# Kernel optimization log

Hardware: AMD Instinct MI355X
Metric: run time of the kernel (lower is better)

The kernel has to match this reference:

```python
import jax, jax.numpy as jnp
import numpy as np

N_TOKENS = 1_000_000
NUM_FEATURES = 128
NUM_CLUSTERS = 64


def setup_inputs() -> dict:
    key = jax.random.key(0)
    kx, kc = jax.random.split(key)
    x = jax.random.normal(kx, (1, N_TOKENS, NUM_FEATURES), dtype=jnp.float32)
    # learned parameter, initialized as torch.randn(num_clusters, num_features)
    cluster_centers = jax.random.normal(kc, (NUM_CLUSTERS, NUM_FEATURES), dtype=jnp.float32)
    return {"x": x, "cluster_centers": cluster_centers}


def reference(x, cluster_centers):
    # x: (1, n, d); cluster_centers: (k, d)
    # O(n*k*d) broadcast intermediate of the original). argmin is identical
    # to argmin over torch.norm since sqrt is monotone.
    x2 = jnp.sum(x * x, axis=-1)                                  # (1, n)
    c2 = jnp.sum(cluster_centers * cluster_centers, axis=-1)      # (k,)
    xc = jnp.einsum('bnd,kd->bnk', x, cluster_centers)            # (1, n, k)
    d2 = x2[..., None] + c2[None, None, :] - 2.0 * xc             # (1, n, k)
    # nearest token index for each cluster (min over the token dim)
    indices = jnp.argmin(d2, axis=1)                              # (1, k)
    # gather the selected token features: (1, k, d)
    selected = x[:, indices[0], :]
    return selected
```

## Files before the change

### kernel.cpp

```cpp
#include <hip/hip_runtime.h>
#include <math.h>

#define NTOK   1000000
#define NFEAT  128
#define NCLUS  64
#define TT     256
#define KC     16
#define NCHUNK (NFEAT / KC)
#define XPAD   260
#define NTILES ((NTOK + TT - 1) / TT)
#define GRID_P 768

__global__ void zero_ctr_kernel(int* ctr) { *ctr = 0; }

__global__ __launch_bounds__(256, 3)
void cluster_part_kernel(const float* __restrict__ x, const float* __restrict__ cc,
                         int* __restrict__ ctr,
                         float* __restrict__ pv, int* __restrict__ pi)
{
    __shared__ float cs[NFEAT][NCLUS];
    __shared__ float xs[KC][XPAD];
    __shared__ float x2s[TT];
    __shared__ float c2s[NCLUS];
    __shared__ int   tileno;

    const int tid = threadIdx.x;
    const int cg  = tid & 7;
    const int tg  = tid >> 3;
    const int l   = tid & 3;
    const int g   = tid >> 2;

    {
        float s = 0.f;
        const float* src = cc + (long)g * NFEAT + l * 4;
        #pragma unroll
        for (int r = 0; r < 8; ++r) {
            float4 v = *(const float4*)(src + r * 16);
            const int f = r * 16 + l * 4;
            cs[f + 0][g] = v.x; cs[f + 1][g] = v.y;
            cs[f + 2][g] = v.z; cs[f + 3][g] = v.w;
            s = fmaf(v.x, v.x, s); s = fmaf(v.y, v.y, s);
            s = fmaf(v.z, v.z, s); s = fmaf(v.w, v.w, s);
        }
        s += __shfl_xor(s, 1);
        s += __shfl_xor(s, 2);
        if (l == 0) c2s[g] = s;
    }
    __syncthreads();

    float c2r[8];
    #pragma unroll
    for (int j = 0; j < 8; ++j) c2r[j] = c2s[cg * 8 + j];

    float bestv[8]; int besti[8];
    #pragma unroll
    for (int j = 0; j < 8; ++j) { bestv[j] = INFINITY; besti[j] = 0x7fffffff; }

    for (;;) {
        if (tid == 0) tileno = atomicAdd(ctr, 1);
        __syncthreads();
        const int tile = tileno;
        if (tile >= NTILES) break;
        const long tb = (long)tile * TT;

        float4 pf[4];
        #pragma unroll
        for (int r = 0; r < 4; ++r) {
            long n = tb + r * 64 + g;
            if (n >= NTOK) n = NTOK - 1;
            pf[r] = *(const float4*)(x + n * NFEAT + l * 4);
        }

        float acc[8][8];
        #pragma unroll
        for (int i = 0; i < 8; ++i)
            #pragma unroll
            for (int j = 0; j < 8; ++j) acc[i][j] = 0.f;
        float x2a[4] = {0.f, 0.f, 0.f, 0.f};

        #pragma unroll 1
        for (int kc = 0; kc < NCHUNK; ++kc) {
            __syncthreads();
            #pragma unroll
            for (int r = 0; r < 4; ++r) {
                float4 v = pf[r];
                const int row = r * 64 + g;
                xs[l * 4 + 0][row] = v.x; xs[l * 4 + 1][row] = v.y;
                xs[l * 4 + 2][row] = v.z; xs[l * 4 + 3][row] = v.w;
                x2a[r] = fmaf(v.x, v.x, x2a[r]);
                x2a[r] = fmaf(v.y, v.y, x2a[r]);
                x2a[r] = fmaf(v.z, v.z, x2a[r]);
                x2a[r] = fmaf(v.w, v.w, x2a[r]);
            }
            if (kc + 1 < NCHUNK) {
                #pragma unroll
                for (int r = 0; r < 4; ++r) {
                    long n = tb + r * 64 + g;
                    if (n >= NTOK) n = NTOK - 1;
                    pf[r] = *(const float4*)(x + n * NFEAT + (kc + 1) * KC + l * 4);
                }
            }
            __syncthreads();

            const int kb = kc * KC;
            #pragma unroll 4
            for (int k = 0; k < KC; ++k) {
                float4 xa = *(const float4*)&xs[k][tg * 8];
                float4 xb = *(const float4*)&xs[k][tg * 8 + 4];
                float4 ca = *(const float4*)&cs[kb + k][cg * 8];
                float4 cb = *(const float4*)&cs[kb + k][cg * 8 + 4];
                float xv[8] = {xa.x, xa.y, xa.z, xa.w, xb.x, xb.y, xb.z, xb.w};
                float cv[8] = {ca.x, ca.y, ca.z, ca.w, cb.x, cb.y, cb.z, cb.w};
                #pragma unroll
                for (int i = 0; i < 8; ++i)
                    #pragma unroll
                    for (int j = 0; j < 8; ++j)
                        acc[i][j] = fmaf(xv[i], cv[j], acc[i][j]);
            }
        }

        #pragma unroll
        for (int r = 0; r < 4; ++r) {
            float s = x2a[r];
            s += __shfl_xor(s, 1);
            s += __shfl_xor(s, 2);
            if (l == 0) x2s[r * 64 + g] = s;
        }
        __syncthreads();

        #pragma unroll
        for (int i = 0; i < 8; ++i) {
            const long n = tb + tg * 8 + i;
            if (n >= NTOK) continue;
            const float x2 = x2s[tg * 8 + i];
            #pragma unroll
            for (int j = 0; j < 8; ++j) {
                float s = (x2 + c2r[j]) - 2.0f * acc[i][j];
                if (s < bestv[j]) { bestv[j] = s; besti[j] = (int)n; }
            }
        }
    }

    __syncthreads();
    float* rv = &xs[0][0];
    int*   ri = (int*)(&xs[0][0] + 2048);
    #pragma unroll
    for (int j = 0; j < 8; ++j) {
        rv[(cg * 8 + j) * 32 + tg] = bestv[j];
        ri[(cg * 8 + j) * 32 + tg] = besti[j];
    }
    __syncthreads();
    if (tid < NCLUS) {
        float bv = rv[tid * 32]; int bi = ri[tid * 32];
        #pragma unroll
        for (int t = 1; t < 32; ++t) {
            float v = rv[tid * 32 + t]; int ii = ri[tid * 32 + t];
            if (v < bv || (v == bv && ii < bi)) { bv = v; bi = ii; }
        }
        pv[(long)blockIdx.x * NCLUS + tid] = bv;
        pi[(long)blockIdx.x * NCLUS + tid] = bi;
    }
}

__global__ __launch_bounds__(256)
void cluster_final_kernel(const float* __restrict__ x,
                          const float* __restrict__ pv, const int* __restrict__ pi,
                          float* __restrict__ out)
{
    const int c   = blockIdx.x;
    const int tid = threadIdx.x;
    __shared__ float sv[256];
    __shared__ int   si[256];

    float bv = INFINITY; int bi = 0x7fffffff;
    for (int b = tid; b < GRID_P; b += 256) {
        float v = pv[(long)b * NCLUS + c]; int ii = pi[(long)b * NCLUS + c];
        if (v < bv || (v == bv && ii < bi)) { bv = v; bi = ii; }
    }
    sv[tid] = bv; si[tid] = bi;
    __syncthreads();
    for (int s = 128; s > 0; s >>= 1) {
        if (tid < s) {
            float v = sv[tid + s]; int ii = si[tid + s];
            if (v < sv[tid] || (v == sv[tid] && ii < si[tid])) {
                sv[tid] = v; si[tid] = ii;
            }
        }
        __syncthreads();
    }
    const int best = si[0];
    if (tid < NFEAT) out[c * NFEAT + tid] = x[(long)best * NFEAT + tid];
}

extern "C" void kernel_launch(void* const* d_in, const int* in_sizes, int n_in,
                              void* d_out, int out_size, void* d_ws, size_t ws_size,
                              hipStream_t stream) {
    const float* x  = (const float*)d_in[0];
    const float* cc = (const float*)d_in[1];
    float* out = (float*)d_out;

    int*   ctr = (int*)d_ws;
    float* pv  = (float*)((char*)d_ws + 256);
    int*   pi  = (int*)((char*)d_ws + 256 + (size_t)GRID_P * NCLUS * sizeof(float));

    zero_ctr_kernel<<<1, 1, 0, stream>>>(ctr);
    cluster_part_kernel<<<GRID_P, 256, 0, stream>>>(x, cc, ctr, pv, pi);
    cluster_final_kernel<<<NCLUS, 256, 0, stream>>>(x, pv, pi, out);
}
```

Baseline: 729.0 us.

## Compute distances with split-bf16 MFMA and per-wave static token partitioning

Replaces the scalar FP32 FMA outer-product GEMM with bf16 MFMA 32x32x16 instructions. Each operand is split into a high and a low bf16 part, and three MFMAs per step approximate FP32 accuracy. Each wave owns 32-token subtiles assigned statically, with register prefetch of x straight from global memory. This removes the atomic tile counter, the LDS staging of x and the block-level barriers. The cost is extra conversion ALU work and a possible argmin mismatch from the reduced-precision dot products, since the lo*lo term is dropped.

```diff
diff --git a/kernel.cpp b/kernel.cpp
--- a/kernel.cpp
+++ b/kernel.cpp
@@ -4,158 +4,153 @@
 #define NTOK   1000000
 #define NFEAT  128
 #define NCLUS  64
-#define TT     256
-#define KC     16
-#define NCHUNK (NFEAT / KC)
-#define XPAD   260
-#define NTILES ((NTOK + TT - 1) / TT)
-#define GRID_P 768
-
-__global__ void zero_ctr_kernel(int* ctr) { *ctr = 0; }
+#define SUBT   32
+#define NSUB   (NTOK / SUBT)
+#define NBLK   768
+#define NWAVE  (NBLK * 4)
+#define CPAD   136
+
+typedef __attribute__((ext_vector_type(8)))  short bf16x8;
+typedef __attribute__((ext_vector_type(16))) float f32x16;
+
+__device__ __forceinline__ unsigned short f2bf(float f) {
+    unsigned u = __float_as_uint(f);
+    return (unsigned short)((u + 0x7fffu + ((u >> 16) & 1u)) >> 16);
+}
+__device__ __forceinline__ float bf2f(unsigned short h) {
+    return __uint_as_float((unsigned)h << 16);
+}
 
 __global__ __launch_bounds__(256, 3)
 void cluster_part_kernel(const float* __restrict__ x, const float* __restrict__ cc,
-                         int* __restrict__ ctr,
                          float* __restrict__ pv, int* __restrict__ pi)
 {
-    __shared__ float cs[NFEAT][NCLUS];
-    __shared__ float xs[KC][XPAD];
-    __shared__ float x2s[TT];
+    __shared__ unsigned short chi[NCLUS][CPAD];
+    __shared__ unsigned short clo[NCLUS][CPAD];
     __shared__ float c2s[NCLUS];
-    __shared__ int   tileno;
+    __shared__ float rv[512];
+    __shared__ int   ri[512];
 
     const int tid = threadIdx.x;
-    const int cg  = tid & 7;
-    const int tg  = tid >> 3;
-    const int l   = tid & 3;
-    const int g   = tid >> 2;
+    const int l   = tid & 63;
+    const int w   = tid >> 6;
+    const int lr  = l & 31;
+    const int lh  = l >> 5;
 
     {
+        const int cl = tid >> 2, q = tid & 3;
+        const float* src = cc + cl * NFEAT + q * 32;
         float s = 0.f;
-        const float* src = cc + (long)g * NFEAT + l * 4;
         #pragma unroll
         for (int r = 0; r < 8; ++r) {
-            float4 v = *(const float4*)(src + r * 16);
-            const int f = r * 16 + l * 4;
-            cs[f + 0][g] = v.x; cs[f + 1][g] = v.y;
-            cs[f + 2][g] = v.z; cs[f + 3][g] = v.w;
-            s = fmaf(v.x, v.x, s); s = fmaf(v.y, v.y, s);
-            s = fmaf(v.z, v.z, s); s = fmaf(v.w, v.w, s);
+            float4 v = *(const float4*)(src + r * 4);
+            float vv[4] = {v.x, v.y, v.z, v.w};
+            #pragma unroll
+            for (int e = 0; e < 4; ++e) {
+                float f = vv[e];
+                unsigned short h  = f2bf(f);
+                unsigned short lo = f2bf(f - bf2f(h));
+                chi[cl][q * 32 + r * 4 + e] = h;
+                clo[cl][q * 32 + r * 4 + e] = lo;
+                s = fmaf(f, f, s);
+            }
         }
         s += __shfl_xor(s, 1);
         s += __shfl_xor(s, 2);
-        if (l == 0) c2s[g] = s;
+        if (q == 0) c2s[cl] = s;
     }
     __syncthreads();
 
-    float c2r[8];
-    #pragma unroll
-    for (int j = 0; j < 8; ++j) c2r[j] = c2s[cg * 8 + j];
-
-    float bestv[8]; int besti[8];
-    #pragma unroll
-    for (int j = 0; j < 8; ++j) { bestv[j] = INFINITY; besti[j] = 0x7fffffff; }
-
-    for (;;) {
-        if (tid == 0) tileno = atomicAdd(ctr, 1);
-        __syncthreads();
-        const int tile = tileno;
-        if (tile >= NTILES) break;
-        const long tb = (long)tile * TT;
-
-        float4 pf[4];
-        #pragma unroll
-        for (int r = 0; r < 4; ++r) {
-            long n = tb + r * 64 + g;
-            if (n >= NTOK) n = NTOK - 1;
-            pf[r] = *(const float4*)(x + n * NFEAT + l * 4);
-        }
-
-        float acc[8][8];
-        #pragma unroll
-        for (int i = 0; i < 8; ++i)
+    const float c2v0 = c2s[lr];
+    const float c2v1 = c2s[lr + 32];
+
+    float bestv0 = INFINITY, bestv1 = INFINITY;
+    int   besti0 = 0x7fffffff, besti1 = 0x7fffffff;
+
+    const int gw = blockIdx.x * 4 + w;
+
+    float4 pfa[2], pfb[2];
+    {
+        const float* p0 = x + ((long)gw * SUBT + lr) * NFEAT + lh * 8;
+        pfa[0] = *(const float4*)(p0);
+        pfb[0] = *(const float4*)(p0 + 4);
+        pfa[1] = *(const float4*)(p0 + 16);
+        pfb[1] = *(const float4*)(p0 + 20);
+    }
+
+    for (int st = gw; st < NSUB; st += NWAVE) {
+        f32x16 acc0, acc1;
+        #pragma unroll
+        for (int i = 0; i < 16; ++i) { acc0[i] = 0.f; acc1[i] = 0.f; }
+        float x2p = 0.f;
+
+        #pragma unroll
+        for (int ks = 0; ks < 8; ++ks) {
+            float4 a = pfa[ks & 1];
+            float4 b = pfb[ks & 1];
+            {
+                const int ks2 = (ks + 2) & 7;
+                const int st2 = (ks < 6) ? st : st + NWAVE;
+                if (st2 < NSUB) {
+                    const float* p2 = x + ((long)st2 * SUBT + lr) * NFEAT + ks2 * 16 + lh * 8;
+                    pfa[ks & 1] = *(const float4*)(p2);
+                    pfb[ks & 1] = *(const float4*)(p2 + 4);
+                }
+            }
+            float av[8] = {a.x, a.y, a.z, a.w, b.x, b.y, b.z, b.w};
+            bf16x8 ahi, alo;
             #pragma unroll
-            for (int j = 0; j < 8; ++j) acc[i][j] = 0.f;
-        float x2a[4] = {0.f, 0.f, 0.f, 0.f};
-
-        #pragma unroll 1
-        for (int kc = 0; kc < NCHUNK; ++kc) {
-            __syncthreads();
+            for (int e = 0; e < 8; ++e) {
+                float f = av[e];
+                unsigned short h  = f2bf(f);
+                unsigned short lo = f2bf(f - bf2f(h));
+                ahi[e] = (short)h;
+                alo[e] = (short)lo;
+                x2p = fmaf(f, f, x2p);
+            }
+            const int ko = ks * 16 + lh * 8;
+            bf16x8 bh0 = *(const bf16x8*)&chi[lr][ko];
+            bf16x8 bh1 = *(const bf16x8*)&chi[lr + 32][ko];
+            bf16x8 bl0 = *(const bf16x8*)&clo[lr][ko];
+            bf16x8 bl1 = *(const bf16x8*)&clo[lr + 32][ko];
+            acc0 = __builtin_amdgcn_mfma_f32_32x32x16_bf16(ahi, bh0, acc0, 0, 0, 0);
+            acc1 = __builtin_amdgcn_mfma_f32_32x32x16_bf16(ahi, bh1, acc1, 0, 0, 0);
+            acc0 = __builtin_amdgcn_mfma_f32_32x32x16_bf16(alo, bh0, acc0, 0, 0, 0);
+            acc1 = __builtin_amdgcn_mfma_f32_32x32x16_bf16(alo, bh1, acc1, 0, 0, 0);
+            acc0 = __builtin_amdgcn_mfma_f32_32x32x16_bf16(ahi, bl0, acc0, 0, 0, 0);
+            acc1 = __builtin_amdgcn_mfma_f32_32x32x16_bf16(ahi, bl1, acc1, 0, 0, 0);
+        }
+
+        const float x2 = x2p + __shfl_xor(x2p, 32);
+
+        const int base = st * SUBT;
+        #pragma unroll
+        for (int reg = 0; reg < 16; ++reg) {
+            const int r    = (reg & 3) + 8 * (reg >> 2) + 4 * lh;
+            const float x2r = __shfl(x2, r);
+            const int n    = base + r;
+            const float d0 = fmaf(-2.f, acc0[reg], x2r + c2v0);
+            const float d1 = fmaf(-2.f, acc1[reg], x2r + c2v1);
+            if (d0 < bestv0 || (d0 == bestv0 && n < besti0)) { bestv0 = d0; besti0 = n; }
+            if (d1 < bestv1 || (d1 == bestv1 && n < besti1)) { bestv1 = d1; besti1 = n; }
+        }
+    }
+
+    rv[(w * 64 + l) * 2 + 0] = bestv0;  ri[(w * 64 + l) * 2 + 0] = besti0;
+    rv[(w * 64 + l) * 2 + 1] = bestv1;  ri[(w * 64 + l) * 2 + 1] = besti1;
+    __syncthreads();
+
+    if (tid < NCLUS) {
+        const int nf = tid >> 5, p = tid & 31;
+        float bv = INFINITY; int bi = 0x7fffffff;
+        #pragma unroll
+        for (int ww = 0; ww < 4; ++ww) {
             #pragma unroll
-            for (int r = 0; r < 4; ++r) {
-                float4 v = pf[r];
-                const int row = r * 64 + g;
-                xs[l * 4 + 0][row] = v.x; xs[l * 4 + 1][row] = v.y;
-                xs[l * 4 + 2][row] = v.z; xs[l * 4 + 3][row] = v.w;
-                x2a[r] = fmaf(v.x, v.x, x2a[r]);
-                x2a[r] = fmaf(v.y, v.y, x2a[r]);
-                x2a[r] = fmaf(v.z, v.z, x2a[r]);
-                x2a[r] = fmaf(v.w, v.w, x2a[r]);
-            }
-            if (kc + 1 < NCHUNK) {
-                #pragma unroll
-                for (int r = 0; r < 4; ++r) {
-                    long n = tb + r * 64 + g;
-                    if (n >= NTOK) n = NTOK - 1;
-                    pf[r] = *(const float4*)(x + n * NFEAT + (kc + 1) * KC + l * 4);
-                }
-            }
-            __syncthreads();
-
-            const int kb = kc * KC;
-            #pragma unroll 4
-            for (int k = 0; k < KC; ++k) {
-                float4 xa = *(const float4*)&xs[k][tg * 8];
-                float4 xb = *(const float4*)&xs[k][tg * 8 + 4];
-                float4 ca = *(const float4*)&cs[kb + k][cg * 8];
-                float4 cb = *(const float4*)&cs[kb + k][cg * 8 + 4];
-                float xv[8] = {xa.x, xa.y, xa.z, xa.w, xb.x, xb.y, xb.z, xb.w};
-                float cv[8] = {ca.x, ca.y, ca.z, ca.w, cb.x, cb.y, cb.z, cb.w};
-                #pragma unroll
-                for (int i = 0; i < 8; ++i)
-                    #pragma unroll
-                    for (int j = 0; j < 8; ++j)
-                        acc[i][j] = fmaf(xv[i], cv[j], acc[i][j]);
-            }
-        }
-
-        #pragma unroll
-        for (int r = 0; r < 4; ++r) {
-            float s = x2a[r];
-            s += __shfl_xor(s, 1);
-            s += __shfl_xor(s, 2);
-            if (l == 0) x2s[r * 64 + g] = s;
-        }
-        __syncthreads();
-
-        #pragma unroll
-        for (int i = 0; i < 8; ++i) {
-            const long n = tb + tg * 8 + i;
-            if (n >= NTOK) continue;
-            const float x2 = x2s[tg * 8 + i];
-            #pragma unroll
-            for (int j = 0; j < 8; ++j) {
-                float s = (x2 + c2r[j]) - 2.0f * acc[i][j];
-                if (s < bestv[j]) { bestv[j] = s; besti[j] = (int)n; }
-            }
-        }
-    }
-
-    __syncthreads();
-    float* rv = &xs[0][0];
-    int*   ri = (int*)(&xs[0][0] + 2048);
-    #pragma unroll
-    for (int j = 0; j < 8; ++j) {
-        rv[(cg * 8 + j) * 32 + tg] = bestv[j];
-        ri[(cg * 8 + j) * 32 + tg] = besti[j];
-    }
-    __syncthreads();
-    if (tid < NCLUS) {
-        float bv = rv[tid * 32]; int bi = ri[tid * 32];
-        #pragma unroll
-        for (int t = 1; t < 32; ++t) {
-            float v = rv[tid * 32 + t]; int ii = ri[tid * 32 + t];
-            if (v < bv || (v == bv && ii < bi)) { bv = v; bi = ii; }
+            for (int hh = 0; hh < 2; ++hh) {
+                const int idx = (ww * 64 + p + hh * 32) * 2 + nf;
+                const float v = rv[idx]; const int ii = ri[idx];
+                if (v < bv || (v == bv && ii < bi)) { bv = v; bi = ii; }
+            }
         }
         pv[(long)blockIdx.x * NCLUS + tid] = bv;
         pi[(long)blockIdx.x * NCLUS + tid] = bi;
@@ -173,7 +168,7 @@
     __shared__ int   si[256];
 
     float bv = INFINITY; int bi = 0x7fffffff;
-    for (int b = tid; b < GRID_P; b += 256) {
+    for (int b = tid; b < NBLK; b += 256) {
         float v = pv[(long)b * NCLUS + c]; int ii = pi[(long)b * NCLUS + c];
         if (v < bv || (v == bv && ii < bi)) { bv = v; bi = ii; }
     }
@@ -199,11 +194,9 @@
     const float* cc = (const float*)d_in[1];
     float* out = (float*)d_out;
 
-    int*   ctr = (int*)d_ws;
-    float* pv  = (float*)((char*)d_ws + 256);
-    int*   pi  = (int*)((char*)d_ws + 256 + (size_t)GRID_P * NCLUS * sizeof(float));
-
-    zero_ctr_kernel<<<1, 1, 0, stream>>>(ctr);
-    cluster_part_kernel<<<GRID_P, 256, 0, stream>>>(x, cc, ctr, pv, pi);
+    float* pv = (float*)d_ws;
+    int*   pi = (int*)((char*)d_ws + (size_t)NBLK * NCLUS * sizeof(float));
+
+    cluster_part_kernel<<<NBLK, 256, 0, stream>>>(x, cc, pv, pi);
     cluster_final_kernel<<<NCLUS, 256, 0, stream>>>(x, pv, pi, out);
 }
```

Result: slower. 756.8 us (+3.8%).
